# Kernel optimization log

Measured on AMD Instinct MI355X. Metric: run time of the kernel, lower is better.

## Reference

```python
import jax, jax.numpy as jnp
import numpy as np

EPS = 1e-5

def _gcn_norm(edge_index, n):
    # Add self-loops, compute symmetric normalization deg^-1/2 * deg^-1/2 (PyG GCNConv).
    src = jnp.concatenate([edge_index[0], jnp.arange(n)])
    dst = jnp.concatenate([edge_index[1], jnp.arange(n)])
    deg = jax.ops.segment_sum(jnp.ones_like(dst, dtype=jnp.float32), dst, num_segments=n)
    dinv = jnp.where(deg > 0, jax.lax.rsqrt(deg), 0.0)
    norm = dinv[src] * dinv[dst]  # [E + N]
    return src, dst, norm

def _gcn_conv(x, W, b, src, dst, norm, n):
    h = x @ W                      # linear first (out_dim < in_dim here)
    msg = h[src] * norm[:, None]   # gather + per-edge scale
    out = jax.ops.segment_sum(msg, dst, num_segments=n)  # scatter-add aggregation
    return out + b

def _bn(x, g, b):
    # BatchNorm over nodes (training-mode batch statistics, biased variance)
    mu = x.mean(axis=0)
    var = jnp.mean((x - mu) ** 2, axis=0)
    return (x - mu) * jax.lax.rsqrt(var + EPS) * g + b


def setup_inputs() -> dict:
    key = jax.random.key(0)
    N, E, F_in = 10000, 320000, 256
    ks = jax.random.split(key, 8)
    dims = [F_in, 220, 150, 100, 60, 17]
    inp = {
        'x': jax.random.normal(ks[0], (N, F_in), dtype=jnp.float32),
        'edge_index': jax.random.randint(ks[1], (2, E), 0, N, dtype=jnp.int64),
    }
    for i in range(5):
        fan_in, fan_out = dims[i], dims[i + 1]
        scale = 1.0 / np.sqrt(fan_in)
        inp[f'W{i+1}'] = jax.random.normal(ks[2 + i], (fan_in, fan_out), dtype=jnp.float32) * scale
        inp[f'b{i+1}'] = jnp.zeros((fan_out,), dtype=jnp.float32)
    for i, d in enumerate([220, 150, 100, 60]):
        inp[f'g{i+1}'] = jnp.ones((d,), dtype=jnp.float32)
        inp[f'be{i+1}'] = jnp.zeros((d,), dtype=jnp.float32)
    return inp


def reference(x, edge_index, W1, b1, W2, b2, W3, b3, W4, b4, W5, b5,
              g1, be1, g2, be2, g3, be3, g4, be4):
    n = x.shape[0]
    src, dst, norm = _gcn_norm(edge_index, n)
    h = _gcn_conv(x, W1, b1, src, dst, norm, n)
    h = _bn(jax.nn.relu(h), g1, be1)
    # dropout omitted (eval-mode identity)
    h = _gcn_conv(h, W2, b2, src, dst, norm, n)
    h = _bn(jax.nn.relu(h), g2, be2)
    h = _gcn_conv(h, W3, b3, src, dst, norm, n)
    h = _bn(jax.nn.relu(h), g3, be3)
    h = _gcn_conv(h, W4, b4, src, dst, norm, n)
    h = _bn(jax.nn.relu(h), g4, be4)
    h = _gcn_conv(h, W5, b5, src, dst, norm, n)
    return jax.nn.log_softmax(h, axis=1)
```

## Files before the change

### kernel.cpp

```cpp
#include <hip/hip_runtime.h>
#include <math.h>

typedef unsigned short ushort_t;
typedef unsigned int uint_t;
typedef unsigned long long ull_t;

__device__ __forceinline__ float bf2f(ushort_t u) {
    union { uint_t i; float f; } x; x.i = ((uint_t)u) << 16; return x.f;
}
__device__ __forceinline__ ushort_t f2bf(float f) {
    union { float f; uint_t i; } x; x.f = f;
    uint_t r = x.i + 0x7FFFu + ((x.i >> 16) & 1u);
    return (ushort_t)(r >> 16);
}

__global__ __launch_bounds__(256) void k_init(
    const float* __restrict__ x, const float* __restrict__ W0,
    int* __restrict__ cnt, float* __restrict__ stats,
    float* __restrict__ wbias, ushort_t* __restrict__ xb, ushort_t* __restrict__ Wt,
    int N)
{
    const int gt = blockIdx.x * 256 + threadIdx.x;
    const int gth = gridDim.x * 256;
    for (int i = gt; i < N; i += gth) cnt[i] = 0;
    for (int i = gt; i < 2048; i += gth) stats[i] = 0.f;
    if (gt < 256) wbias[gt] = 0.f;
    const int n4 = N * 64;
    for (int i = gt; i < n4; i += gth) {
        float4 v = ((const float4*)x)[i];
        ushort_t* o = xb + i * 4;
        o[0] = f2bf(v.x); o[1] = f2bf(v.y); o[2] = f2bf(v.z); o[3] = f2bf(v.w);
    }
    for (int idx = gt; idx < 224 * 256; idx += gth) {
        int j = idx >> 8;
        int k = idx & 255;
        float v = (j < 220) ? W0[(long)k * 220 + j] : 0.f;
        Wt[idx] = f2bf(v);
    }
}

__global__ void k_hist(const int* __restrict__ dst, int* __restrict__ cnt, int E) {
    int e = blockIdx.x * blockDim.x + threadIdx.x;
    if (e < E) atomicAdd(&cnt[dst[e]], 1);
}

__global__ __launch_bounds__(1024) void k_scan(
    const int* __restrict__ cnt, int* __restrict__ row_start,
    int* __restrict__ cursor, float* __restrict__ dinv, int N)
{
    __shared__ int sh[1024];
    const int tid = threadIdx.x;
    const int chunk = (N + 1023) >> 10;
    int loc[16];
    const int base = tid * chunk;
    int sum = 0;
    for (int c = 0; c < chunk; ++c) {
        int i = base + c;
        int v = (i < N) ? cnt[i] : 0;
        loc[c] = sum;
        sum += v;
    }
    sh[tid] = sum;
    __syncthreads();
    for (int off = 1; off < 1024; off <<= 1) {
        int v = (tid >= off) ? sh[tid - off] : 0;
        __syncthreads();
        sh[tid] += v;
        __syncthreads();
    }
    const int excl = sh[tid] - sum;
    for (int c = 0; c < chunk; ++c) {
        int i = base + c;
        if (i < N) {
            int rs = excl + loc[c];
            row_start[i] = rs;
            cursor[i] = rs;
            dinv[i] = rsqrtf(1.0f + (float)cnt[i]);
        }
    }
    if (tid == 1023) row_start[N] = sh[1023];
}

__global__ void k_fill(const int* __restrict__ src, const int* __restrict__ dst,
                       int* __restrict__ cursor, int* __restrict__ csr_src, int E) {
    int e = blockIdx.x * blockDim.x + threadIdx.x;
    if (e < E) {
        int pos = atomicAdd(&cursor[dst[e]], 1);
        csr_src[pos] = src[e];
    }
}

__global__ void k_prep(const float* __restrict__ W,
                       const float* __restrict__ g, const float* __restrict__ be,
                       const float* __restrict__ cs, const float* __restrict__ cq,
                       ushort_t* __restrict__ Wt, float* __restrict__ wbias,
                       int K, int M, int Kp, int Mp, int yW, float invN)
{
    __shared__ float sm[256];
    if ((int)blockIdx.y < yW) {
        if (threadIdx.y == 0) {
            int kk = blockIdx.x * 64 + threadIdx.x;
            float sc = 0.f;
            if (kk < K) {
                float mu = cs[kk] * invN;
                float var = cq[kk] * invN - mu * mu;
                sc = g[kk] * rsqrtf(var + 1e-5f);
            }
            sm[threadIdx.x] = sc;
        }
        __syncthreads();
        int k = blockIdx.x * 64 + threadIdx.x;
        int j = blockIdx.y * 4 + threadIdx.y;
        if (k >= Kp || j >= Mp) return;
        float v = 0.f;
        if (k < K && j < M) v = sm[threadIdx.x] * W[(long)k * M + j];
        Wt[(long)j * Kp + k] = f2bf(v);
    } else {
        __shared__ float red[4][64];
        int t = threadIdx.y * 64 + threadIdx.x;
        for (int kk = t; kk < K; kk += 256) {
            float mu = cs[kk] * invN;
            float var = cq[kk] * invN - mu * mu;
            float sc = g[kk] * rsqrtf(var + 1e-5f);
            sm[kk] = be[kk] - mu * sc;
        }
        __syncthreads();
        int jl = t & 63, kg = t >> 6;
        int j = blockIdx.x * 64 + jl;
        float s = 0.f;
        if (j < M) {
            for (int k = kg; k < K; k += 4) s += sm[k] * W[(long)k * M + j];
        }
        red[kg][jl] = s;
        __syncthreads();
        if (kg == 0 && j < Mp) wbias[j] = red[0][jl] + red[1][jl] + red[2][jl] + red[3][jl];
    }
}

template<int KP>
__global__ __launch_bounds__(256) void k_gemm_mfma(
    const ushort_t* __restrict__ Xb, const ushort_t* __restrict__ Wt,
    const float* __restrict__ wbias, const float* __restrict__ dinv,
    ushort_t* __restrict__ h2, int N, int Mp)
{
    typedef __attribute__((ext_vector_type(8))) short short8;
    typedef __attribute__((ext_vector_type(4))) float floatx4;
    constexpr int LSTR = KP + 16;
    __shared__ ushort_t Bs[64 * LSTR];

    const int tid = threadIdx.x;
    const int wave = tid >> 6, lane = tid & 63;
    const int m = lane & 15, quad = lane >> 4;
    const int i0 = blockIdx.x * 64 + wave * 16;
    const int j0 = blockIdx.y * 64;
    const int ncols = min(64, Mp - j0);
    const int ntiles = ncols >> 4;

    {
        const int cpr = KP / 8;
        const int chunks = ncols * cpr;
        for (int c = tid; c < chunks; c += 256) {
            int jj = c / cpr;
            int kk = (c - jj * cpr) * 8;
            *(short8*)(Bs + jj * LSTR + kk) =
                *(const short8*)(Wt + (long)(j0 + jj) * KP + kk);
        }
    }
    __syncthreads();

    if (i0 >= N) return;

    floatx4 acc[4];
    #pragma unroll
    for (int t = 0; t < 4; ++t) { acc[t].x = 0.f; acc[t].y = 0.f; acc[t].z = 0.f; acc[t].w = 0.f; }

    const int ra = min(i0 + m, N - 1);
    const ushort_t* arow = Xb + (long)ra * KP + quad * 8;

    #pragma unroll
    for (int k0 = 0; k0 < KP; k0 += 32) {
        short8 av = *(const short8*)(arow + k0);
        #pragma unroll
        for (int t = 0; t < 4; ++t) {
            if (t < ntiles) {
                short8 bv = *(const short8*)(Bs + (t * 16 + m) * LSTR + k0 + quad * 8);
                acc[t] = __builtin_amdgcn_mfma_f32_16x16x32_bf16(av, bv, acc[t], 0, 0, 0);
            }
        }
    }

    #pragma unroll
    for (int t = 0; t < 4; ++t) {
        if (t < ntiles) {
            int j = j0 + t * 16 + m;
            float wb = wbias[j];
            #pragma unroll
            for (int r = 0; r < 4; ++r) {
                int i = i0 + quad * 4 + r;
                if (i < N) h2[(long)i * Mp + j] = f2bf((acc[t][r] + wb) * dinv[i]);
            }
        }
    }
}

__global__ __launch_bounds__(256) void k_agg(
    const int* __restrict__ row_start, const int* __restrict__ csr_src,
    const ushort_t* __restrict__ h2, int hs,
    const float* __restrict__ dinv, const float* __restrict__ b,
    ushort_t* __restrict__ tmpb, int ts,
    int N, int M, int Q, ull_t magic, uint_t sh)
{
    const uint_t g = blockIdx.x * 256 + threadIdx.x;
    const uint_t i = (uint_t)(((ull_t)g * magic) >> sh);
    const int jp = (int)(g - i * Q);
    if (i >= (uint_t)N) return;
    const int j0 = jp * 4;
    if (j0 >= M) {
        *(uint2*)(tmpb + (long)i * ts + j0) = make_uint2(0u, 0u);
        return;
    }
    const int s0 = row_start[i];
    const int s1 = row_start[i + 1];
    const ushort_t* hp = h2 + j0;
    uint2 v = *(const uint2*)(hp + (long)i * hs);
    float a0 = bf2f((ushort_t)(v.x & 0xffff)), a1 = bf2f((ushort_t)(v.x >> 16));
    float a2 = bf2f((ushort_t)(v.y & 0xffff)), a3 = bf2f((ushort_t)(v.y >> 16));
    int e = s0;
    for (; e + 3 < s1; e += 4) {
        int n0 = csr_src[e], n1 = csr_src[e + 1], n2 = csr_src[e + 2], n3 = csr_src[e + 3];
        uint2 w0 = *(const uint2*)(hp + (long)n0 * hs);
        uint2 w1 = *(const uint2*)(hp + (long)n1 * hs);
        uint2 w2 = *(const uint2*)(hp + (long)n2 * hs);
        uint2 w3 = *(const uint2*)(hp + (long)n3 * hs);
        a0 += bf2f((ushort_t)(w0.x & 0xffff)); a1 += bf2f((ushort_t)(w0.x >> 16));
        a2 += bf2f((ushort_t)(w0.y & 0xffff)); a3 += bf2f((ushort_t)(w0.y >> 16));
        a0 += bf2f((ushort_t)(w1.x & 0xffff)); a1 += bf2f((ushort_t)(w1.x >> 16));
        a2 += bf2f((ushort_t)(w1.y & 0xffff)); a3 += bf2f((ushort_t)(w1.y >> 16));
        a0 += bf2f((ushort_t)(w2.x & 0xffff)); a1 += bf2f((ushort_t)(w2.x >> 16));
        a2 += bf2f((ushort_t)(w2.y & 0xffff)); a3 += bf2f((ushort_t)(w2.y >> 16));
        a0 += bf2f((ushort_t)(w3.x & 0xffff)); a1 += bf2f((ushort_t)(w3.x >> 16));
        a2 += bf2f((ushort_t)(w3.y & 0xffff)); a3 += bf2f((ushort_t)(w3.y >> 16));
    }
    for (; e < s1; ++e) {
        uint2 w = *(const uint2*)(hp + (long)csr_src[e] * hs);
        a0 += bf2f((ushort_t)(w.x & 0xffff)); a1 += bf2f((ushort_t)(w.x >> 16));
        a2 += bf2f((ushort_t)(w.y & 0xffff)); a3 += bf2f((ushort_t)(w.y >> 16));
    }
    const float di = dinv[i];
    float r0 = (j0     < M) ? fmaxf(a0 * di + b[j0],     0.f) : 0.f;
    float r1 = (j0 + 1 < M) ? fmaxf(a1 * di + b[j0 + 1], 0.f) : 0.f;
    float r2 = (j0 + 2 < M) ? fmaxf(a2 * di + b[j0 + 2], 0.f) : 0.f;
    float r3 = (j0 + 3 < M) ? fmaxf(a3 * di + b[j0 + 3], 0.f) : 0.f;
    uint2 pk;
    pk.x = (uint_t)f2bf(r0) | ((uint_t)f2bf(r1) << 16);
    pk.y = (uint_t)f2bf(r2) | ((uint_t)f2bf(r3) << 16);
    *(uint2*)(tmpb + (long)i * ts + j0) = pk;
}

__global__ __launch_bounds__(256) void k_stats(
    const ushort_t* __restrict__ tmpb, int ts,
    float* __restrict__ cs, float* __restrict__ csq, int N)
{
    const int t = threadIdx.x;
    if (2 * t >= ts) return;
    const int i0 = blockIdx.x * 64;
    float s0 = 0.f, q0 = 0.f, s1 = 0.f, q1 = 0.f;
    for (int r = 0; r < 64; ++r) {
        int i = i0 + r;
        if (i < N) {
            uint_t w = *(const uint_t*)(tmpb + (long)i * ts + 2 * t);
            float v0 = bf2f((ushort_t)(w & 0xffff));
            float v1 = bf2f((ushort_t)(w >> 16));
            s0 += v0; q0 += v0 * v0;
            s1 += v1; q1 += v1 * v1;
        }
    }
    atomicAdd(&cs[2 * t], s0);
    atomicAdd(&csq[2 * t], q0);
    atomicAdd(&cs[2 * t + 1], s1);
    atomicAdd(&csq[2 * t + 1], q1);
}

__global__ __launch_bounds__(256) void k_agg_final(
    const int* __restrict__ row_start, const int* __restrict__ csr_src,
    const ushort_t* __restrict__ h2, const float* __restrict__ dinv,
    const float* __restrict__ b, float* __restrict__ out, int N, int M)
{
    const int x = threadIdx.x;
    const int i = blockIdx.x * 16 + threadIdx.y;
    if (i >= N) return;
    const int j0 = 2 * x, j1 = 2 * x + 1;
    uint_t v = *(const uint_t*)(h2 + (long)i * 32 + j0);
    float a0 = bf2f((ushort_t)(v & 0xffff));
    float a1 = bf2f((ushort_t)(v >> 16));
    const int s0 = row_start[i];
    const int s1 = row_start[i + 1];
    int e = s0;
    for (; e + 1 < s1; e += 2) {
        int n0 = csr_src[e], n1 = csr_src[e + 1];
        uint_t w0 = *(const uint_t*)(h2 + (long)n0 * 32 + j0);
        uint_t w1 = *(const uint_t*)(h2 + (long)n1 * 32 + j0);
        a0 += bf2f((ushort_t)(w0 & 0xffff)); a1 += bf2f((ushort_t)(w0 >> 16));
        a0 += bf2f((ushort_t)(w1 & 0xffff)); a1 += bf2f((ushort_t)(w1 >> 16));
    }
    for (; e < s1; ++e) {
        uint_t w = *(const uint_t*)(h2 + (long)csr_src[e] * 32 + j0);
        a0 += bf2f((ushort_t)(w & 0xffff)); a1 += bf2f((ushort_t)(w >> 16));
    }
    const float di = dinv[i];
    float r0 = (j0 < M) ? (a0 * di + b[j0]) : -INFINITY;
    float r1 = (j1 < M) ? (a1 * di + b[j1]) : -INFINITY;
    float m = fmaxf(r0, r1);
    #pragma unroll
    for (int msk = 1; msk < 16; msk <<= 1) m = fmaxf(m, __shfl_xor(m, msk, 16));
    float s = ((j0 < M) ? expf(r0 - m) : 0.f) + ((j1 < M) ? expf(r1 - m) : 0.f);
    #pragma unroll
    for (int msk = 1; msk < 16; msk <<= 1) s += __shfl_xor(s, msk, 16);
    const float l = logf(s) + m;
    if (j0 < M) out[(long)i * M + j0] = r0 - l;
    if (j1 < M) out[(long)i * M + j1] = r1 - l;
}


static inline int pad16(int v) { return (v + 15) & ~15; }
static inline int pad32(int v) { return (v + 31) & ~31; }

extern "C" void kernel_launch(void* const* d_in, const int* in_sizes, int n_in,
                              void* d_out, int out_size, void* d_ws, size_t ws_size,
                              hipStream_t stream)
{
    const int dims[6] = {256, 220, 150, 100, 60, 17};
    const int N = in_sizes[0] / dims[0];
    const int E = in_sizes[1] / 2;

    const float* x  = (const float*)d_in[0];
    const int* ei   = (const int*)d_in[1];
    const int* srcv = ei;
    const int* dstv = ei + E;
    const float* Wl[5], *bl[5];
    for (int l = 0; l < 5; ++l) {
        Wl[l] = (const float*)d_in[2 + 2 * l];
        bl[l] = (const float*)d_in[3 + 2 * l];
    }
    const float* gl[4], *bel[4];
    for (int l = 0; l < 4; ++l) {
        gl[l]  = (const float*)d_in[12 + 2 * l];
        bel[l] = (const float*)d_in[13 + 2 * l];
    }
    float* out = (float*)d_out;

    char* w = (char*)d_ws;
    const long NB  = ((long)N * 4 + 255) & ~255L;
    const long NB1 = ((long)(N + 1) * 4 + 255) & ~255L;
    const long EB  = ((long)E * 4 + 255) & ~255L;
    const long XBB = ((long)N * 256 * 2 + 255) & ~255L;
    const long FBB = ((long)N * 224 * 2 + 255) & ~255L;
    const long WTB = ((long)224 * 256 * 2 + 255) & ~255L;

    long o = 0;
    float* dinv      = (float*)(w + o);  o += NB;
    float* stats     = (float*)(w + o);  o += 2048 * 4;
    float* wbias     = (float*)(w + o);  o += 1024;
    int*   cnt       = (int*)(w + o);    o += NB;
    int*   row_start = (int*)(w + o);    o += NB1;
    int*   cursor    = (int*)(w + o);    o += NB;
    int*   csr_src   = (int*)(w + o);    o += EB;
    ushort_t* xb     = (ushort_t*)(w + o); o += XBB;
    ushort_t* Wt     = (ushort_t*)(w + o); o += WTB;
    ushort_t* h2     = (ushort_t*)(w + o); o += FBB;
    ushort_t* tmpb   = (ushort_t*)(w + o); o += FBB;

    const int eBlk = (E + 255) / 256;
    const float invN = 1.0f / (float)N;

    k_init<<<(N * 64 + 255) / 256, 256, 0, stream>>>(x, Wl[0], cnt, stats,
                                                     wbias, xb, Wt, N);
    k_hist<<<eBlk, 256, 0, stream>>>(dstv, cnt, E);
    k_scan<<<1, 1024, 0, stream>>>(cnt, row_start, cursor, dinv, N);
    k_fill<<<eBlk, 256, 0, stream>>>(srcv, dstv, cursor, csr_src, E);

    for (int l = 0; l < 5; ++l) {
        const int K  = dims[l];
        const int M  = dims[l + 1];
        const int Kp = pad32(K);
        const int Mp = pad16(M);
        const int ts = (l < 4) ? pad32(M) : 32;
        const ushort_t* X = (l == 0) ? xb : tmpb;

        if (l > 0) {
            const int yW = (Mp + 3) / 4;
            k_prep<<<dim3((Kp + 63) / 64, yW + 1), dim3(64, 4), 0, stream>>>(
                Wl[l], gl[l - 1], bel[l - 1],
                stats + (l - 1) * 512, stats + (l - 1) * 512 + 256,
                Wt, wbias, K, M, Kp, Mp, yW, invN);
        }

        dim3 gg((N + 63) / 64, (Mp + 63) / 64);
        switch (Kp) {
            case 256: k_gemm_mfma<256><<<gg, 256, 0, stream>>>(X, Wt, wbias, dinv, h2, N, Mp); break;
            case 224: k_gemm_mfma<224><<<gg, 256, 0, stream>>>(X, Wt, wbias, dinv, h2, N, Mp); break;
            case 160: k_gemm_mfma<160><<<gg, 256, 0, stream>>>(X, Wt, wbias, dinv, h2, N, Mp); break;
            case 128: k_gemm_mfma<128><<<gg, 256, 0, stream>>>(X, Wt, wbias, dinv, h2, N, Mp); break;
            case  64: k_gemm_mfma< 64><<<gg, 256, 0, stream>>>(X, Wt, wbias, dinv, h2, N, Mp); break;
        }

        if (l < 4) {
            const int Q = ts / 4;
            uint_t shmt = 0;
            while ((1u << shmt) < (uint_t)Q) ++shmt;
            shmt += 32;
            const ull_t magic = ((1ULL << shmt) + Q - 1) / (ull_t)Q;
            const long total = (long)N * Q;
            k_agg<<<(int)((total + 255) / 256), 256, 0, stream>>>(
                row_start, csr_src, h2, Mp, dinv, bl[l], tmpb, ts, N, M, Q, magic, shmt);
            k_stats<<<(N + 63) / 64, 256, 0, stream>>>(tmpb, ts,
                stats + l * 512, stats + l * 512 + 256, N);
        } else {
            k_agg_final<<<(N + 15) / 16, dim3(16, 16), 0, stream>>>(
                row_start, csr_src, h2, dinv, bl[l], out, N, M);
        }
    }
}
```

Before: 406.9 us.

## Fuse fp32-to-bf16 input conversion into first GEMM and widen aggregation vectors

Drops the separate pass that converts x to bf16 in the init kernel. The first-layer GEMM now reads fp32 rows directly and converts them to bf16 in registers, which saves a full write and re-read of the bf16 copy of x. The aggregation kernel now handles 8 features per thread with 16-byte gathers instead of 4 with 8-byte gathers. That halves the thread count and the repeated CSR index loads, at the cost of more registers per thread and less parallelism. The W0 transpose moves into its own small kernel.

Result: no change. 400.6 us (-1.5%).

```diff
diff --git a/kernel.cpp b/kernel.cpp
--- a/kernel.cpp
+++ b/kernel.cpp
@@ -15,22 +15,20 @@
 }
 
 __global__ __launch_bounds__(256) void k_init(
-    const float* __restrict__ x, const float* __restrict__ W0,
-    int* __restrict__ cnt, float* __restrict__ stats,
-    float* __restrict__ wbias, ushort_t* __restrict__ xb, ushort_t* __restrict__ Wt,
-    int N)
+    int* __restrict__ cnt, float* __restrict__ stats, float* __restrict__ wbias, int N)
 {
     const int gt = blockIdx.x * 256 + threadIdx.x;
     const int gth = gridDim.x * 256;
     for (int i = gt; i < N; i += gth) cnt[i] = 0;
     for (int i = gt; i < 2048; i += gth) stats[i] = 0.f;
     if (gt < 256) wbias[gt] = 0.f;
-    const int n4 = N * 64;
-    for (int i = gt; i < n4; i += gth) {
-        float4 v = ((const float4*)x)[i];
-        ushort_t* o = xb + i * 4;
-        o[0] = f2bf(v.x); o[1] = f2bf(v.y); o[2] = f2bf(v.z); o[3] = f2bf(v.w);
-    }
+}
+
+__global__ __launch_bounds__(256) void k_prep0(
+    const float* __restrict__ W0, ushort_t* __restrict__ Wt)
+{
+    const int gt = blockIdx.x * 256 + threadIdx.x;
+    const int gth = gridDim.x * 256;
     for (int idx = gt; idx < 224 * 256; idx += gth) {
         int j = idx >> 8;
         int k = idx & 255;
@@ -137,9 +135,9 @@
     }
 }
 
-template<int KP>
+template<int KP, bool F32A>
 __global__ __launch_bounds__(256) void k_gemm_mfma(
-    const ushort_t* __restrict__ Xb, const ushort_t* __restrict__ Wt,
+    const void* __restrict__ Xin, const ushort_t* __restrict__ Wt,
     const float* __restrict__ wbias, const float* __restrict__ dinv,
     ushort_t* __restrict__ h2, int N, int Mp)
 {
@@ -175,11 +173,22 @@
     for (int t = 0; t < 4; ++t) { acc[t].x = 0.f; acc[t].y = 0.f; acc[t].z = 0.f; acc[t].w = 0.f; }
 
     const int ra = min(i0 + m, N - 1);
-    const ushort_t* arow = Xb + (long)ra * KP + quad * 8;
+    const ushort_t* arow_h = F32A ? nullptr : (const ushort_t*)Xin + (long)ra * KP + quad * 8;
+    const float*    arow_f = F32A ? (const float*)Xin + (long)ra * KP + quad * 8 : nullptr;
 
     #pragma unroll
     for (int k0 = 0; k0 < KP; k0 += 32) {
-        short8 av = *(const short8*)(arow + k0);
+        short8 av;
+        if (F32A) {
+            float4 f0 = *(const float4*)(arow_f + k0);
+            float4 f1 = *(const float4*)(arow_f + k0 + 4);
+            av[0] = (short)f2bf(f0.x); av[1] = (short)f2bf(f0.y);
+            av[2] = (short)f2bf(f0.z); av[3] = (short)f2bf(f0.w);
+            av[4] = (short)f2bf(f1.x); av[5] = (short)f2bf(f1.y);
+            av[6] = (short)f2bf(f1.z); av[7] = (short)f2bf(f1.w);
+        } else {
+            av = *(const short8*)(arow_h + k0);
+        }
         #pragma unroll
         for (int t = 0; t < 4; ++t) {
             if (t < ntiles) {
@@ -214,47 +223,66 @@
     const uint_t i = (uint_t)(((ull_t)g * magic) >> sh);
     const int jp = (int)(g - i * Q);
     if (i >= (uint_t)N) return;
-    const int j0 = jp * 4;
+    const int j0 = jp * 8;
     if (j0 >= M) {
-        *(uint2*)(tmpb + (long)i * ts + j0) = make_uint2(0u, 0u);
+        *(uint4*)(tmpb + (long)i * ts + j0) = make_uint4(0u, 0u, 0u, 0u);
         return;
     }
     const int s0 = row_start[i];
     const int s1 = row_start[i + 1];
     const ushort_t* hp = h2 + j0;
-    uint2 v = *(const uint2*)(hp + (long)i * hs);
-    float a0 = bf2f((ushort_t)(v.x & 0xffff)), a1 = bf2f((ushort_t)(v.x >> 16));
-    float a2 = bf2f((ushort_t)(v.y & 0xffff)), a3 = bf2f((ushort_t)(v.y >> 16));
+    float acc[8];
+    {
+        uint4 v = *(const uint4*)(hp + (long)i * hs);
+        acc[0] = bf2f((ushort_t)(v.x & 0xffff)); acc[1] = bf2f((ushort_t)(v.x >> 16));
+        acc[2] = bf2f((ushort_t)(v.y & 0xffff)); acc[3] = bf2f((ushort_t)(v.y >> 16));
+        acc[4] = bf2f((ushort_t)(v.z & 0xffff)); acc[5] = bf2f((ushort_t)(v.z >> 16));
+        acc[6] = bf2f((ushort_t)(v.w & 0xffff)); acc[7] = bf2f((ushort_t)(v.w >> 16));
+    }
     int e = s0;
     for (; e + 3 < s1; e += 4) {
         int n0 = csr_src[e], n1 = csr_src[e + 1], n2 = csr_src[e + 2], n3 = csr_src[e + 3];
-        uint2 w0 = *(const uint2*)(hp + (long)n0 * hs);
-        uint2 w1 = *(const uint2*)(hp + (long)n1 * hs);
-        uint2 w2 = *(const uint2*)(hp + (long)n2 * hs);
-        uint2 w3 = *(const uint2*)(hp + (long)n3 * hs);
-        a0 += bf2f((ushort_t)(w0.x & 0xffff)); a1 += bf2f((ushort_t)(w0.x >> 16));
-        a2 += bf2f((ushort_t)(w0.y & 0xffff)); a3 += bf2f((ushort_t)(w0.y >> 16));
-        a0 += bf2f((ushort_t)(w1.x & 0xffff)); a1 += bf2f((ushort_t)(w1.x >> 16));
-        a2 += bf2f((ushort_t)(w1.y & 0xffff)); a3 += bf2f((ushort_t)(w1.y >> 16));
-        a0 += bf2f((ushort_t)(w2.x & 0xffff)); a1 += bf2f((ushort_t)(w2.x >> 16));
-        a2 += bf2f((ushort_t)(w2.y & 0xffff)); a3 += bf2f((ushort_t)(w2.y >> 16));
-        a0 += bf2f((ushort_t)(w3.x & 0xffff)); a1 += bf2f((ushort_t)(w3.x >> 16));
-        a2 += bf2f((ushort_t)(w3.y & 0xffff)); a3 += bf2f((ushort_t)(w3.y >> 16));
+        uint4 w0 = *(const uint4*)(hp + (long)n0 * hs);
+        uint4 w1 = *(const uint4*)(hp + (long)n1 * hs);
+        uint4 w2 = *(const uint4*)(hp + (long)n2 * hs);
+        uint4 w3 = *(const uint4*)(hp + (long)n3 * hs);
+        acc[0] += bf2f((ushort_t)(w0.x & 0xffff)); acc[1] += bf2f((ushort_t)(w0.x >> 16));
+        acc[2] += bf2f((ushort_t)(w0.y & 0xffff)); acc[3] += bf2f((ushort_t)(w0.y >> 16));
+        acc[4] += bf2f((ushort_t)(w0.z & 0xffff)); acc[5] += bf2f((ushort_t)(w0.z >> 16));
+        acc[6] += bf2f((ushort_t)(w0.w & 0xffff)); acc[7] += bf2f((ushort_t)(w0.w >> 16));
+        acc[0] += bf2f((ushort_t)(w1.x & 0xffff)); acc[1] += bf2f((ushort_t)(w1.x >> 16));
+        acc[2] += bf2f((ushort_t)(w1.y & 0xffff)); acc[3] += bf2f((ushort_t)(w1.y >> 16));
+        acc[4] += bf2f((ushort_t)(w1.z & 0xffff)); acc[5] += bf2f((ushort_t)(w1.z >> 16));
+        acc[6] += bf2f((ushort_t)(w1.w & 0xffff)); acc[7] += bf2f((ushort_t)(w1.w >> 16));
+        acc[0] += bf2f((ushort_t)(w2.x & 0xffff)); acc[1] += bf2f((ushort_t)(w2.x >> 16));
+        acc[2] += bf2f((ushort_t)(w2.y & 0xffff)); acc[3] += bf2f((ushort_t)(w2.y >> 16));
+        acc[4] += bf2f((ushort_t)(w2.z & 0xffff)); acc[5] += bf2f((ushort_t)(w2.z >> 16));
+        acc[6] += bf2f((ushort_t)(w2.w & 0xffff)); acc[7] += bf2f((ushort_t)(w2.w >> 16));
+        acc[0] += bf2f((ushort_t)(w3.x & 0xffff)); acc[1] += bf2f((ushort_t)(w3.x >> 16));
+        acc[2] += bf2f((ushort_t)(w3.y & 0xffff)); acc[3] += bf2f((ushort_t)(w3.y >> 16));
+        acc[4] += bf2f((ushort_t)(w3.z & 0xffff)); acc[5] += bf2f((ushort_t)(w3.z >> 16));
+        acc[6] += bf2f((ushort_t)(w3.w & 0xffff)); acc[7] += bf2f((ushort_t)(w3.w >> 16));
     }
     for (; e < s1; ++e) {
-        uint2 w = *(const uint2*)(hp + (long)csr_src[e] * hs);
-        a0 += bf2f((ushort_t)(w.x & 0xffff)); a1 += bf2f((ushort_t)(w.x >> 16));
-        a2 += bf2f((ushort_t)(w.y & 0xffff)); a3 += bf2f((ushort_t)(w.y >> 16));
+        uint4 w = *(const uint4*)(hp + (long)csr_src[e] * hs);
+        acc[0] += bf2f((ushort_t)(w.x & 0xffff)); acc[1] += bf2f((ushort_t)(w.x >> 16));
+        acc[2] += bf2f((ushort_t)(w.y & 0xffff)); acc[3] += bf2f((ushort_t)(w.y >> 16));
+        acc[4] += bf2f((ushort_t)(w.z & 0xffff)); acc[5] += bf2f((ushort_t)(w.z >> 16));
+        acc[6] += bf2f((ushort_t)(w.w & 0xffff)); acc[7] += bf2f((ushort_t)(w.w >> 16));
     }
     const float di = dinv[i];
-    float r0 = (j0     < M) ? fmaxf(a0 * di + b[j0],     0.f) : 0.f;
-    float r1 = (j0 + 1 < M) ? fmaxf(a1 * di + b[j0 + 1], 0.f) : 0.f;
-    float r2 = (j0 + 2 < M) ? fmaxf(a2 * di + b[j0 + 2], 0.f) : 0.f;
-    float r3 = (j0 + 3 < M) ? fmaxf(a3 * di + b[j0 + 3], 0.f) : 0.f;
-    uint2 pk;
-    pk.x = (uint_t)f2bf(r0) | ((uint_t)f2bf(r1) << 16);
-    pk.y = (uint_t)f2bf(r2) | ((uint_t)f2bf(r3) << 16);
-    *(uint2*)(tmpb + (long)i * ts + j0) = pk;
+    ushort_t r[8];
+    #pragma unroll
+    for (int u = 0; u < 8; ++u) {
+        float v = (j0 + u < M) ? fmaxf(acc[u] * di + b[j0 + u], 0.f) : 0.f;
+        r[u] = f2bf(v);
+    }
+    uint4 pk;
+    pk.x = (uint_t)r[0] | ((uint_t)r[1] << 16);
+    pk.y = (uint_t)r[2] | ((uint_t)r[3] << 16);
+    pk.z = (uint_t)r[4] | ((uint_t)r[5] << 16);
+    pk.w = (uint_t)r[6] | ((uint_t)r[7] << 16);
+    *(uint4*)(tmpb + (long)i * ts + j0) = pk;
 }
 
 __global__ __launch_bounds__(256) void k_stats(
@@ -353,7 +381,6 @@
     const long NB  = ((long)N * 4 + 255) & ~255L;
     const long NB1 = ((long)(N + 1) * 4 + 255) & ~255L;
     const long EB  = ((long)E * 4 + 255) & ~255L;
-    const long XBB = ((long)N * 256 * 2 + 255) & ~255L;
     const long FBB = ((long)N * 224 * 2 + 255) & ~255L;
     const long WTB = ((long)224 * 256 * 2 + 255) & ~255L;
 
@@ -365,7 +392,6 @@
     int*   row_start = (int*)(w + o);    o += NB1;
     int*   cursor    = (int*)(w + o);    o += NB;
     int*   csr_src   = (int*)(w + o);    o += EB;
-    ushort_t* xb     = (ushort_t*)(w + o); o += XBB;
     ushort_t* Wt     = (ushort_t*)(w + o); o += WTB;
     ushort_t* h2     = (ushort_t*)(w + o); o += FBB;
     ushort_t* tmpb   = (ushort_t*)(w + o); o += FBB;
@@ -373,8 +399,8 @@
     const int eBlk = (E + 255) / 256;
     const float invN = 1.0f / (float)N;
 
-    k_init<<<(N * 64 + 255) / 256, 256, 0, stream>>>(x, Wl[0], cnt, stats,
-                                                     wbias, xb, Wt, N);
+    k_init<<<(N + 255) / 256, 256, 0, stream>>>(cnt, stats, wbias, N);
+    k_prep0<<<56, 256, 0, stream>>>(Wl[0], Wt);
     k_hist<<<eBlk, 256, 0, stream>>>(dstv, cnt, E);
     k_scan<<<1, 1024, 0, stream>>>(cnt, row_start, cursor, dinv, N);
     k_fill<<<eBlk, 256, 0, stream>>>(srcv, dstv, cursor, csr_src, E);
@@ -385,7 +411,6 @@
         const int Kp = pad32(K);
         const int Mp = pad16(M);
         const int ts = (l < 4) ? pad32(M) : 32;
-        const ushort_t* X = (l == 0) ? xb : tmpb;
 
         if (l > 0) {
             const int yW = (Mp + 3) / 4;
@@ -396,16 +421,19 @@
         }
 
         dim3 gg((N + 63) / 64, (Mp + 63) / 64);
-        switch (Kp) {
-            case 256: k_gemm_mfma<256><<<gg, 256, 0, stream>>>(X, Wt, wbias, dinv, h2, N, Mp); break;
-            case 224: k_gemm_mfma<224><<<gg, 256, 0, stream>>>(X, Wt, wbias, dinv, h2, N, Mp); break;
-            case 160: k_gemm_mfma<160><<<gg, 256, 0, stream>>>(X, Wt, wbias, dinv, h2, N, Mp); break;
-            case 128: k_gemm_mfma<128><<<gg, 256, 0, stream>>>(X, Wt, wbias, dinv, h2, N, Mp); break;
-            case  64: k_gemm_mfma< 64><<<gg, 256, 0, stream>>>(X, Wt, wbias, dinv, h2, N, Mp); break;
+        if (l == 0) {
+            k_gemm_mfma<256, true><<<gg, 256, 0, stream>>>(x, Wt, wbias, dinv, h2, N, Mp);
+        } else {
+            switch (Kp) {
+                case 224: k_gemm_mfma<224, false><<<gg, 256, 0, stream>>>(tmpb, Wt, wbias, dinv, h2, N, Mp); break;
+                case 160: k_gemm_mfma<160, false><<<gg, 256, 0, stream>>>(tmpb, Wt, wbias, dinv, h2, N, Mp); break;
+                case 128: k_gemm_mfma<128, false><<<gg, 256, 0, stream>>>(tmpb, Wt, wbias, dinv, h2, N, Mp); break;
+                case  64: k_gemm_mfma< 64, false><<<gg, 256, 0, stream>>>(tmpb, Wt, wbias, dinv, h2, N, Mp); break;
+            }
         }
 
         if (l < 4) {
-            const int Q = ts / 4;
+            const int Q = ts / 8;
             uint_t shmt = 0;
             while ((1u << shmt) < (uint_t)Q) ++shmt;
             shmt += 32;
```
